# Kernel optimization log

Hardware: AMD Instinct MI355X
Metric: run time of the kernel (lower is better)

## Reference

```python
import jax, jax.numpy as jnp
import numpy as np

L = 4096
E = 512   # embed dim
S = 1024  # state dim
H = 150   # Scorer hidden dim
GI = 2 * S + E
MAX_N = 10


def _scorer(x, W1, b1, W2, b2, W3, b3):
    h = jax.nn.relu(x @ W1 + b1)
    h = jax.nn.relu(h @ W2 + b2)
    return h @ W3 + b3  # [..., 1]


def setup_inputs() -> dict:
    key = jax.random.key(0)
    ks = jax.random.split(key, 16)
    def init(k, shape, fan_in):
        return jax.random.normal(k, shape, dtype=jnp.float32) / np.sqrt(fan_in)
    inp = {
        "embeds": jax.random.normal(ks[0], (L, E), dtype=jnp.float32),
        "states": jax.random.normal(ks[1], (L, S), dtype=jnp.float32),
        # attention Scorer params (input S)
        "aW1": init(ks[2], (S, H), S), "ab1": jnp.zeros((H,), jnp.float32),
        "aW2": init(ks[3], (H, H), H), "ab2": jnp.zeros((H,), jnp.float32),
        "aW3": init(ks[4], (H, 1), H), "ab3": jnp.zeros((1,), jnp.float32),
        # sm Scorer params (input GI)
        "sW1": init(ks[5], (GI, H), GI), "sb1": jnp.zeros((H,), jnp.float32),
        "sW2": init(ks[6], (H, H), H), "sb2": jnp.zeros((H,), jnp.float32),
        "sW3": init(ks[7], (H, 1), H), "sb3": jnp.zeros((1,), jnp.float32),
    }
    return inp


def reference(embeds, states, aW1, ab1, aW2, ab2, aW3, ab3,
              sW1, sb1, sW2, sb2, sW3, sb3):
    # per-token attention logits, computed once: [L]
    attns = _scorer(states, aW1, ab1, aW2, ab2, aW3, ab3)[:, 0]

    gs = []
    for n in range(1, MAX_N + 1):  # fixed small loop over window sizes
        M = L - n + 1                                  # number of windows
        starts = jnp.arange(M)
        idx = starts[:, None] + jnp.arange(n)          # [M, n] token indices
        w = jax.nn.softmax(attns[idx], axis=1)         # windowed softmax [M, n]
        pooled = jnp.einsum('mn,mne->me', w, embeds[idx])  # [M, E]
        g = jnp.concatenate([states[starts], states[starts + n - 1], pooled],
                            axis=1)                    # [M, 2S+E]
        gs.append(g)
    x = jnp.concatenate(gs, axis=0)                    # [T, GI], T = 10L-45
    scores = _scorer(x, sW1, sb1, sW2, sb2, sW3, sb3)[:, 0]  # [T]
    return scores
```

## Files before the change

kernel.cpp:

```cpp
#include <hip/hip_runtime.h>
#include <math.h>

#define LTOK 4096
#define EDIM 512
#define SDIM 1024
#define HDIM 150
#define SEG 160
#define MAXN 10
#define TOTAL_ROWS 40915
#define KA 1536
#define NKT 48
#define K2 160
#define NCG 42

typedef _Float16 hfrag __attribute__((ext_vector_type(8)));
typedef float ffrag __attribute__((ext_vector_type(4)));


#define ITEMS_A   (LTOK * (KA / 8))
#define ITEMS_W   (NCG * NKT * 64)
#define ITEMS_W2  (K2 * (K2 / 8))
#define ITEMS_A2  (K2 * (K2 / 8))
#define ITEMS_TOT (ITEMS_A + ITEMS_W + ITEMS_W2 + ITEMS_A2)

__global__ __launch_bounds__(256) void prep_kernel(
    const float* __restrict__ embeds, const float* __restrict__ states,
    const float* __restrict__ aW1, const float* __restrict__ aW2,
    const float* __restrict__ sW1, const float* __restrict__ sW2,
    _Float16* __restrict__ Apk, _Float16* __restrict__ Wpk,
    _Float16* __restrict__ W2pk, _Float16* __restrict__ A2pk)
{
    int it = blockIdx.x * 256 + threadIdx.x;
    if (it < ITEMS_A) {
        const int rem = it % (NKT * 64);
        const int g = it / (NKT * 64), kt = rem >> 6, lane = rem & 63;
        const int row = g * 16 + (lane & 15);
        const int k0 = kt * 32 + (lane >> 4) * 8;
        const float* src = (k0 < SDIM) ? (states + (size_t)row * SDIM + k0)
                                       : (embeds + (size_t)row * EDIM + (k0 - SDIM));
        const float4 v0 = *(const float4*)src;
        const float4 v1 = *(const float4*)(src + 4);
        _Float16 o[8] = {(_Float16)v0.x, (_Float16)v0.y, (_Float16)v0.z, (_Float16)v0.w,
                         (_Float16)v1.x, (_Float16)v1.y, (_Float16)v1.z, (_Float16)v1.w};
        *(uint4*)(Apk + (size_t)it * 8) = *(uint4*)o;
        return;
    }
    it -= ITEMS_A;
    if (it < ITEMS_W) {
        const int rem = it % (NKT * 64);
        const int cgi = it / (NKT * 64), kt = rem >> 6, lane = rem & 63;
        const int col = cgi * 16 + (lane & 15);
        const int k0 = kt * 32 + (lane >> 4) * 8;
        _Float16 o[8];
        for (int j = 0; j < 8; ++j) {
            const int k = k0 + j;
            float wv = 0.f;
            if (col < 160) {
                if (col < HDIM && k < SDIM) wv = sW1[(size_t)k * HDIM + col];
            } else if (col < 320) {
                const int cj = col - 160;
                if (cj < HDIM && k < SDIM) wv = sW1[(size_t)(SDIM + k) * HDIM + cj];
            } else if (col < 480) {
                const int cj = col - 320;
                if (cj < HDIM && k >= SDIM) wv = sW1[(size_t)(SDIM + k) * HDIM + cj];
            } else if (col >= 512) {
                const int cj = col - 512;
                if (cj < HDIM && k < SDIM) wv = aW1[(size_t)k * HDIM + cj];
            }
            o[j] = (_Float16)wv;
        }
        *(uint4*)(Wpk + ((size_t)((size_t)cgi * NKT + kt) * 64 + lane) * 8) = *(uint4*)o;
        return;
    }
    it -= ITEMS_W;
    if (it < ITEMS_W2 + ITEMS_A2) {
        const bool is_a = (it >= ITEMS_W2);
        const int li = is_a ? (it - ITEMS_W2) : it;
        const float* src = is_a ? aW2 : sW2;
        _Float16* dst = is_a ? A2pk : W2pk;
        const int tk = li >> 6, lane = li & 63;
        const int col = (tk / 5) * 16 + (lane & 15);
        const int k0 = (tk % 5) * 32 + (lane >> 4) * 8;
        _Float16 o[8];
        for (int j = 0; j < 8; ++j) {
            const int k = k0 + j;
            float wv = (col < HDIM && k < HDIM) ? src[(size_t)k * HDIM + col] : 0.f;
            o[j] = (_Float16)wv;
        }
        *(uint4*)(dst + ((size_t)tk * 64 + lane) * 8) = *(uint4*)o;
    }
}

__global__ __launch_bounds__(256) void k_proj(
    const _Float16* __restrict__ Apk, const _Float16* __restrict__ Wpk,
    const _Float16* __restrict__ A2pk,
    const float* __restrict__ ab1, const float* __restrict__ ab2,
    const float* __restrict__ aW3, const float* __restrict__ ab3,
    _Float16* __restrict__ P1h, _Float16* __restrict__ P2h,
    _Float16* __restrict__ PEh, float* __restrict__ attns)
{
    const int bid = blockIdx.x;
    const int tid = threadIdx.x;
    const int w = tid >> 6, lane = tid & 63;
    const int quad = lane >> 4, l16 = lane & 15;

    __shared__ __align__(16) _Float16 smem[64 * SEG];

    if (bid % 9 == 0) {
        _Float16* ah1 = smem;
        const int tok0 = (bid / 9) * 64;
        const int g = tok0 / 16 + w;

        ffrag acc[10];
#pragma unroll
        for (int c = 0; c < 10; ++c) acc[c] = (ffrag){0.f, 0.f, 0.f, 0.f};

        const _Float16* ap = Apk + ((size_t)g * NKT) * 512 + lane * 8;
#pragma unroll 2
        for (int kt = 0; kt < 32; ++kt) {
            const hfrag a = *(const hfrag*)(ap + (size_t)kt * 512);
#pragma unroll
            for (int c = 0; c < 10; ++c) {
                const hfrag b = *(const hfrag*)(
                    Wpk + (((size_t)(32 + c) * NKT + kt) * 64 + lane) * 8);
                acc[c] = __builtin_amdgcn_mfma_f32_16x16x32_f16(a, b, acc[c], 0, 0, 0);
            }
        }
#pragma unroll
        for (int c = 0; c < 10; ++c) {
            const int col = c * 16 + l16;
            const float b1 = (col < HDIM) ? ab1[col] : 0.f;
#pragma unroll
            for (int r = 0; r < 4; ++r) {
                const int row = w * 16 + quad * 4 + r;
                ah1[row * SEG + col] = (_Float16)fmaxf(acc[c][r] + b1, 0.f);
            }
        }
        __syncthreads();

        hfrag af[5];
#pragma unroll
        for (int ks = 0; ks < 5; ++ks)
            af[ks] = *(const hfrag*)&ah1[(w * 16 + l16) * SEG + ks * 32 + quad * 8];

        float part[4] = {0.f, 0.f, 0.f, 0.f};
        for (int ct = 0; ct < 10; ++ct) {
            ffrag a2 = (ffrag){0.f, 0.f, 0.f, 0.f};
#pragma unroll
            for (int ks = 0; ks < 5; ++ks) {
                const hfrag fb = *(const hfrag*)(
                    A2pk + ((size_t)(ct * 5 + ks) * 64 + lane) * 8);
                a2 = __builtin_amdgcn_mfma_f32_16x16x32_f16(af[ks], fb, a2, 0, 0, 0);
            }
            const int col = ct * 16 + l16;
            const float s2 = (col < HDIM) ? ab2[col] : 0.f;
            const float s3 = (col < HDIM) ? aW3[col] : 0.f;
#pragma unroll
            for (int r = 0; r < 4; ++r) part[r] += fmaxf(a2[r] + s2, 0.f) * s3;
        }
#pragma unroll
        for (int off = 1; off < 16; off <<= 1) {
#pragma unroll
            for (int r = 0; r < 4; ++r) part[r] += __shfl_xor(part[r], off, 64);
        }
        if (l16 == 0) {
            const float b3 = ab3[0];
#pragma unroll
            for (int r = 0; r < 4; ++r)
                attns[tok0 + w * 16 + quad * 4 + r] = part[r] + b3;
        }
        return;
    }

    const int tile = bid - bid / 9 - 1;
    const int bM = tile & 63, bN = tile >> 6;
    const int wm = w & 1, wn = w >> 1;
    const int gbase0 = bM * 4;
    const int cgbase0 = bN * 4;
    const int cgbase = cgbase0 + wn * 2;
    const bool alive = (cgbase < 30);
    const int kt0 = (bN >= 5) ? 32 : 0;
    const int kt1 = (bN >= 5) ? 48 : 32;

    _Float16* As = smem;
    _Float16* Bs = smem + 4096;

    const int sgrp = tid >> 6, sln = tid & 63;
    const _Float16* aSrc = Apk + (((size_t)(gbase0 + sgrp) * NKT) * 64 + sln) * 8;
    const _Float16* bSrc = Wpk + (((size_t)(cgbase0 + sgrp) * NKT) * 64 + sln) * 8;
    const int sOff = (sgrp * 64 + sln) * 8;

    ffrag acc[2][2];
#pragma unroll
    for (int t = 0; t < 2; ++t)
#pragma unroll
        for (int u = 0; u < 2; ++u) acc[t][u] = (ffrag){0.f, 0.f, 0.f, 0.f};

    const int aOff0 = ((wm * 2 + 0) * 64 + lane) * 8;
    const int aOff1 = ((wm * 2 + 1) * 64 + lane) * 8;
    const int bOff0 = ((wn * 2 + 0) * 64 + lane) * 8;
    const int bOff1 = ((wn * 2 + 1) * 64 + lane) * 8;

    {
        const uint4 va = *(const uint4*)(aSrc + (size_t)kt0 * 512);
        const uint4 vb = *(const uint4*)(bSrc + (size_t)kt0 * 512);
        *(uint4*)(As + sOff) = va;
        *(uint4*)(Bs + sOff) = vb;
    }
    uint4 qa, qb;
    if (kt0 + 1 < kt1) {
        qa = *(const uint4*)(aSrc + (size_t)(kt0 + 1) * 512);
        qb = *(const uint4*)(bSrc + (size_t)(kt0 + 1) * 512);
    }
    __syncthreads();

    int buf = 0;
    for (int kt = kt0; kt < kt1; ++kt) {
        uint4 na, nb;
        const bool have2 = (kt + 2 < kt1);
        const bool have1 = (kt + 1 < kt1);
        if (have2) {
            na = *(const uint4*)(aSrc + (size_t)(kt + 2) * 512);
            nb = *(const uint4*)(bSrc + (size_t)(kt + 2) * 512);
        }
        if (have1) {
            *(uint4*)(As + (buf ^ 1) * 2048 + sOff) = qa;
            *(uint4*)(Bs + (buf ^ 1) * 2048 + sOff) = qb;
        }
        const _Float16* Ab = As + buf * 2048;
        const _Float16* Bb = Bs + buf * 2048;
        const hfrag a0 = *(const hfrag*)(Ab + aOff0);
        const hfrag a1 = *(const hfrag*)(Ab + aOff1);
        const hfrag b0 = *(const hfrag*)(Bb + bOff0);
        const hfrag b1 = *(const hfrag*)(Bb + bOff1);
        acc[0][0] = __builtin_amdgcn_mfma_f32_16x16x32_f16(a0, b0, acc[0][0], 0, 0, 0);
        acc[1][0] = __builtin_amdgcn_mfma_f32_16x16x32_f16(a1, b0, acc[1][0], 0, 0, 0);
        acc[0][1] = __builtin_amdgcn_mfma_f32_16x16x32_f16(a0, b1, acc[0][1], 0, 0, 0);
        acc[1][1] = __builtin_amdgcn_mfma_f32_16x16x32_f16(a1, b1, acc[1][1], 0, 0, 0);
        __syncthreads();
        qa = na; qb = nb;
        buf ^= 1;
    }

    if (alive) {
#pragma unroll
        for (int t = 0; t < 2; ++t)
#pragma unroll
            for (int u = 0; u < 2; ++u) {
                const int col = (cgbase + u) * 16 + l16;
#pragma unroll
                for (int r = 0; r < 4; ++r) {
                    const int row = (gbase0 + wm * 2 + t) * 16 + quad * 4 + r;
                    const _Float16 hv = (_Float16)acc[t][u][r];
                    if (col < 160)      P1h[(size_t)row * SEG + col] = hv;
                    else if (col < 320) P2h[(size_t)row * SEG + (col - 160)] = hv;
                    else if (col < 480) PEh[(size_t)row * SEG + (col - 320)] = hv;
                }
            }
    }
}

__global__ __launch_bounds__(256) void span_kernel(
    const float* __restrict__ attns, const _Float16* __restrict__ P1h,
    const _Float16* __restrict__ P2h, const _Float16* __restrict__ PEh,
    const float* __restrict__ sb1, const _Float16* __restrict__ W2pk,
    const float* __restrict__ sb2, const float* __restrict__ sW3,
    const float* __restrict__ sb3, float* __restrict__ out)
{
    const int pairI = blockIdx.x % 5;
    const int mChunk = blockIdx.x / 5;
    const int n0 = 2 * pairI + 1, n1 = n0 + 1;
    const int Mn0 = LTOK - n0 + 1, Mn1 = Mn0 - 1;
    const int m0 = mChunk * 32;
    const int offn0 = (n0 - 1) * LTOK - ((n0 - 1) * (n0 - 2)) / 2;
    const int offn1 = offn0 + Mn0;

    const int tid = threadIdx.x;
    const int w = tid >> 6, lane = tid & 63, quad = lane >> 4, l16 = lane & 15;

    __shared__ __align__(16) _Float16 h1h[2][32 * K2];
    __shared__ float wgt[2][32][MAXN];

    if (tid < 64) {
        const int q = tid >> 5, r = tid & 31;
        const int n = q ? n1 : n0;
        const int Mn = q ? Mn1 : Mn0;
        const int m = m0 + r;
        if (m < Mn) {
            float av[MAXN];
#pragma unroll
            for (int j = 0; j < MAXN; ++j)
                av[j] = attns[min(m + j, LTOK - 1)];
            float mx = -1e30f;
            for (int j = 0; j < n; ++j) mx = fmaxf(mx, av[j]);
            float tp[MAXN]; float s = 0.f;
            for (int j = 0; j < n; ++j) { tp[j] = expf(av[j] - mx); s += tp[j]; }
            const float inv = 1.f / s;
            for (int j = 0; j < MAXN; ++j) wgt[q][r][j] = (j < n) ? tp[j] * inv : 0.f;
        } else {
            for (int j = 0; j < MAXN; ++j) wgt[q][r][j] = 0.f;
        }
    }
    __syncthreads();

    for (int item = tid; item < 32 * (K2 / 8); item += 256) {
        const int r = item / (K2 / 8), cc = item % (K2 / 8);
        const int c0 = cc * 8;
        const int mm = m0 + r;
        const hfrag p1  = *(const hfrag*)(P1h + (size_t)mm * SEG + c0);
        const hfrag p2a = *(const hfrag*)(P2h + (size_t)min(mm + n0 - 1, LTOK - 1) * SEG + c0);
        const hfrag p2b = *(const hfrag*)(P2h + (size_t)min(mm + n0, LTOK - 1) * SEG + c0);
        float b1v[8];
#pragma unroll
        for (int e = 0; e < 8; ++e)
            b1v[e] = (c0 + e < HDIM) ? sb1[c0 + e] : 0.f;
        float a0[8], a1[8];
#pragma unroll
        for (int e = 0; e < 8; ++e) {
            a0[e] = (float)p1[e] + (float)p2a[e] + b1v[e];
            a1[e] = (float)p1[e] + (float)p2b[e] + b1v[e];
        }
#pragma unroll
        for (int j = 0; j < MAXN; ++j) {
            const int mj = min(mm + j, LTOK - 1);
            const hfrag pe = *(const hfrag*)(PEh + (size_t)mj * SEG + c0);
            const float w0j = wgt[0][r][j];
            const float w1j = wgt[1][r][j];
#pragma unroll
            for (int e = 0; e < 8; ++e) {
                const float pv = (float)pe[e];
                a0[e] = fmaf(w0j, pv, a0[e]);
                a1[e] = fmaf(w1j, pv, a1[e]);
            }
        }
        _Float16 o0[8], o1[8];
#pragma unroll
        for (int e = 0; e < 8; ++e) {
            const bool live = (c0 + e < HDIM);
            o0[e] = live ? (_Float16)fmaxf(a0[e], 0.f) : (_Float16)0.f;
            o1[e] = live ? (_Float16)fmaxf(a1[e], 0.f) : (_Float16)0.f;
        }
        *(uint4*)&h1h[0][r * K2 + c0] = *(uint4*)o0;
        *(uint4*)&h1h[1][r * K2 + c0] = *(uint4*)o1;
    }
    __syncthreads();

    const int q = w >> 1, rg = w & 1;
    const int Mq = q ? Mn1 : Mn0;
    const int offq = q ? offn1 : offn0;

    hfrag af[5];
#pragma unroll
    for (int ks = 0; ks < 5; ++ks)
        af[ks] = *(const hfrag*)&h1h[q][(rg * 16 + l16) * K2 + ks * 32 + quad * 8];

    float part[4] = {0.f, 0.f, 0.f, 0.f};
    for (int ct = 0; ct < 10; ++ct) {
        ffrag acc = (ffrag){0.f, 0.f, 0.f, 0.f};
#pragma unroll
        for (int ks = 0; ks < 5; ++ks) {
            const hfrag fb = *(const hfrag*)(
                W2pk + ((size_t)(ct * 5 + ks) * 64 + lane) * 8);
            acc = __builtin_amdgcn_mfma_f32_16x16x32_f16(af[ks], fb, acc, 0, 0, 0);
        }
        const int col = ct * 16 + l16;
        const float s2 = (col < HDIM) ? sb2[col] : 0.f;
        const float s3 = (col < HDIM) ? sW3[col] : 0.f;
#pragma unroll
        for (int r = 0; r < 4; ++r) part[r] += fmaxf(acc[r] + s2, 0.f) * s3;
    }

#pragma unroll
    for (int off = 1; off < 16; off <<= 1) {
#pragma unroll
        for (int r = 0; r < 4; ++r) part[r] += __shfl_xor(part[r], off, 64);
    }
    if (l16 == 0) {
        const float b3 = sb3[0];
#pragma unroll
        for (int r = 0; r < 4; ++r) {
            const int lr = rg * 16 + quad * 4 + r;
            if (m0 + lr < Mq) out[offq + m0 + lr] = part[r] + b3;
        }
    }
}

extern "C" void kernel_launch(void* const* d_in, const int* in_sizes, int n_in,
                              void* d_out, int out_size, void* d_ws, size_t ws_size,
                              hipStream_t stream) {
    const float* embeds = (const float*)d_in[0];
    const float* states = (const float*)d_in[1];
    const float* aW1 = (const float*)d_in[2];
    const float* ab1 = (const float*)d_in[3];
    const float* aW2 = (const float*)d_in[4];
    const float* ab2 = (const float*)d_in[5];
    const float* aW3 = (const float*)d_in[6];
    const float* ab3 = (const float*)d_in[7];
    const float* sW1 = (const float*)d_in[8];
    const float* sb1 = (const float*)d_in[9];
    const float* sW2 = (const float*)d_in[10];
    const float* sb2 = (const float*)d_in[11];
    const float* sW3 = (const float*)d_in[12];
    const float* sb3 = (const float*)d_in[13];
    float* out = (float*)d_out;

    float* attns = (float*)d_ws;
    _Float16* P1h  = (_Float16*)(attns + LTOK);
    _Float16* P2h  = P1h + (size_t)LTOK * SEG;
    _Float16* PEh  = P2h + (size_t)LTOK * SEG;
    _Float16* Apk  = PEh + (size_t)LTOK * SEG;
    _Float16* Wpk  = Apk + (size_t)ITEMS_A * 8;
    _Float16* W2pk = Wpk + (size_t)ITEMS_W * 8;
    _Float16* A2pk = W2pk + (size_t)ITEMS_W2 * 8;

    prep_kernel<<<ITEMS_TOT / 256, 256, 0, stream>>>(
        embeds, states, aW1, aW2, sW1, sW2, Apk, Wpk, W2pk, A2pk);
    k_proj<<<576, 256, 0, stream>>>(
        Apk, Wpk, A2pk, ab1, ab2, aW3, ab3, P1h, P2h, PEh, attns);
    span_kernel<<<640, 256, 0, stream>>>(
        attns, P1h, P2h, PEh, sb1, W2pk, sb2, sW3, sb3, out);
}
```

Measured before the change: 145.9 us.

## Fuse activation fp16 conversion into projection GEMM and stage PE rows in LDS

Drops the pre-packing of states/embeds into an fp16 MFMA layout in prep_kernel. The projection kernel now reads fp32 activations directly and converts them to fp16 while loading its tiles, which removes a full write and re-read of the packed activation buffer. The span kernel also stages the 41 PE rows each block needs into shared memory, so the 10-tap window sum reads LDS instead of repeated global loads. In exchange the GEMM loads twice the bytes per A fragment from global memory, with less coalesced strided row reads, and the span kernel uses more shared memory, which may lower occupancy.

```diff
diff --git a/kernel.cpp b/kernel.cpp
--- a/kernel.cpp
+++ b/kernel.cpp
@@ -17,35 +17,18 @@
 typedef float ffrag __attribute__((ext_vector_type(4)));
 
 
-#define ITEMS_A   (LTOK * (KA / 8))
 #define ITEMS_W   (NCG * NKT * 64)
 #define ITEMS_W2  (K2 * (K2 / 8))
 #define ITEMS_A2  (K2 * (K2 / 8))
-#define ITEMS_TOT (ITEMS_A + ITEMS_W + ITEMS_W2 + ITEMS_A2)
+#define ITEMS_PREP (ITEMS_W + ITEMS_W2 + ITEMS_A2)
 
 __global__ __launch_bounds__(256) void prep_kernel(
-    const float* __restrict__ embeds, const float* __restrict__ states,
     const float* __restrict__ aW1, const float* __restrict__ aW2,
     const float* __restrict__ sW1, const float* __restrict__ sW2,
-    _Float16* __restrict__ Apk, _Float16* __restrict__ Wpk,
-    _Float16* __restrict__ W2pk, _Float16* __restrict__ A2pk)
+    _Float16* __restrict__ Wpk, _Float16* __restrict__ W2pk,
+    _Float16* __restrict__ A2pk)
 {
     int it = blockIdx.x * 256 + threadIdx.x;
-    if (it < ITEMS_A) {
-        const int rem = it % (NKT * 64);
-        const int g = it / (NKT * 64), kt = rem >> 6, lane = rem & 63;
-        const int row = g * 16 + (lane & 15);
-        const int k0 = kt * 32 + (lane >> 4) * 8;
-        const float* src = (k0 < SDIM) ? (states + (size_t)row * SDIM + k0)
-                                       : (embeds + (size_t)row * EDIM + (k0 - SDIM));
-        const float4 v0 = *(const float4*)src;
-        const float4 v1 = *(const float4*)(src + 4);
-        _Float16 o[8] = {(_Float16)v0.x, (_Float16)v0.y, (_Float16)v0.z, (_Float16)v0.w,
-                         (_Float16)v1.x, (_Float16)v1.y, (_Float16)v1.z, (_Float16)v1.w};
-        *(uint4*)(Apk + (size_t)it * 8) = *(uint4*)o;
-        return;
-    }
-    it -= ITEMS_A;
     if (it < ITEMS_W) {
         const int rem = it % (NKT * 64);
         const int cgi = it / (NKT * 64), kt = rem >> 6, lane = rem & 63;
@@ -92,8 +75,8 @@
 }
 
 __global__ __launch_bounds__(256) void k_proj(
-    const _Float16* __restrict__ Apk, const _Float16* __restrict__ Wpk,
-    const _Float16* __restrict__ A2pk,
+    const float* __restrict__ states, const float* __restrict__ embeds,
+    const _Float16* __restrict__ Wpk, const _Float16* __restrict__ A2pk,
     const float* __restrict__ ab1, const float* __restrict__ ab2,
     const float* __restrict__ aW3, const float* __restrict__ ab3,
     _Float16* __restrict__ P1h, _Float16* __restrict__ P2h,
@@ -109,16 +92,21 @@
     if (bid % 9 == 0) {
         _Float16* ah1 = smem;
         const int tok0 = (bid / 9) * 64;
-        const int g = tok0 / 16 + w;
 
         ffrag acc[10];
 #pragma unroll
         for (int c = 0; c < 10; ++c) acc[c] = (ffrag){0.f, 0.f, 0.f, 0.f};
 
-        const _Float16* ap = Apk + ((size_t)g * NKT) * 512 + lane * 8;
+        const float* ap = states + (size_t)(tok0 + w * 16 + l16) * SDIM + quad * 8;
 #pragma unroll 2
         for (int kt = 0; kt < 32; ++kt) {
-            const hfrag a = *(const hfrag*)(ap + (size_t)kt * 512);
+            const float4 v0 = *(const float4*)(ap + kt * 32);
+            const float4 v1 = *(const float4*)(ap + kt * 32 + 4);
+            hfrag a;
+            a[0] = (_Float16)v0.x; a[1] = (_Float16)v0.y;
+            a[2] = (_Float16)v0.z; a[3] = (_Float16)v0.w;
+            a[4] = (_Float16)v1.x; a[5] = (_Float16)v1.y;
+            a[6] = (_Float16)v1.z; a[7] = (_Float16)v1.w;
 #pragma unroll
             for (int c = 0; c < 10; ++c) {
                 const hfrag b = *(const hfrag*)(
@@ -186,7 +174,10 @@
     _Float16* Bs = smem + 4096;
 
     const int sgrp = tid >> 6, sln = tid & 63;
-    const _Float16* aSrc = Apk + (((size_t)(gbase0 + sgrp) * NKT) * 64 + sln) * 8;
+    const int srow = (gbase0 + sgrp) * 16 + (sln & 15);
+    const int skcol = (sln >> 4) * 8;
+    const float* aRowS = states + (size_t)srow * SDIM;
+    const float* aRowE = embeds + (size_t)srow * EDIM;
     const _Float16* bSrc = Wpk + (((size_t)(cgbase0 + sgrp) * NKT) * 64 + sln) * 8;
     const int sOff = (sgrp * 64 + sln) * 8;
 
@@ -201,30 +192,46 @@
     const int bOff0 = ((wn * 2 + 0) * 64 + lane) * 8;
     const int bOff1 = ((wn * 2 + 1) * 64 + lane) * 8;
 
+#define A_LOAD(kt, d0, d1)                                                  \
+    {                                                                       \
+        const int k0_ = (kt) * 32 + skcol;                                  \
+        const float* s_ = (k0_ < SDIM) ? (aRowS + k0_)                      \
+                                       : (aRowE + (k0_ - SDIM));            \
+        d0 = *(const float4*)s_;                                            \
+        d1 = *(const float4*)(s_ + 4);                                      \
+    }
+#define A_STORE(buf_, d0, d1)                                               \
+    {                                                                       \
+        _Float16 o_[8] = {(_Float16)d0.x, (_Float16)d0.y, (_Float16)d0.z,   \
+                          (_Float16)d0.w, (_Float16)d1.x, (_Float16)d1.y,   \
+                          (_Float16)d1.z, (_Float16)d1.w};                  \
+        *(uint4*)(As + (buf_) * 2048 + sOff) = *(uint4*)o_;                 \
+    }
+
     {
-        const uint4 va = *(const uint4*)(aSrc + (size_t)kt0 * 512);
-        const uint4 vb = *(const uint4*)(bSrc + (size_t)kt0 * 512);
-        *(uint4*)(As + sOff) = va;
-        *(uint4*)(Bs + sOff) = vb;
-    }
-    uint4 qa, qb;
+        float4 p0, p1;
+        A_LOAD(kt0, p0, p1);
+        A_STORE(0, p0, p1);
+        *(uint4*)(Bs + sOff) = *(const uint4*)(bSrc + (size_t)kt0 * 512);
+    }
+    float4 qa0, qa1; uint4 qb;
     if (kt0 + 1 < kt1) {
-        qa = *(const uint4*)(aSrc + (size_t)(kt0 + 1) * 512);
+        A_LOAD(kt0 + 1, qa0, qa1);
         qb = *(const uint4*)(bSrc + (size_t)(kt0 + 1) * 512);
     }
     __syncthreads();
 
     int buf = 0;
     for (int kt = kt0; kt < kt1; ++kt) {
-        uint4 na, nb;
+        float4 na0, na1; uint4 nb;
         const bool have2 = (kt + 2 < kt1);
         const bool have1 = (kt + 1 < kt1);
         if (have2) {
-            na = *(const uint4*)(aSrc + (size_t)(kt + 2) * 512);
+            A_LOAD(kt + 2, na0, na1);
             nb = *(const uint4*)(bSrc + (size_t)(kt + 2) * 512);
         }
         if (have1) {
-            *(uint4*)(As + (buf ^ 1) * 2048 + sOff) = qa;
+            A_STORE(buf ^ 1, qa0, qa1);
             *(uint4*)(Bs + (buf ^ 1) * 2048 + sOff) = qb;
         }
         const _Float16* Ab = As + buf * 2048;
@@ -238,9 +245,11 @@
         acc[0][1] = __builtin_amdgcn_mfma_f32_16x16x32_f16(a0, b1, acc[0][1], 0, 0, 0);
         acc[1][1] = __builtin_amdgcn_mfma_f32_16x16x32_f16(a1, b1, acc[1][1], 0, 0, 0);
         __syncthreads();
-        qa = na; qb = nb;
+        qa0 = na0; qa1 = na1; qb = nb;
         buf ^= 1;
     }
+#undef A_LOAD
+#undef A_STORE
 
     if (alive) {
 #pragma unroll
@@ -279,7 +288,15 @@
     const int w = tid >> 6, lane = tid & 63, quad = lane >> 4, l16 = lane & 15;
 
     __shared__ __align__(16) _Float16 h1h[2][32 * K2];
+    __shared__ __align__(16) _Float16 PEs[41 * SEG];
     __shared__ float wgt[2][32][MAXN];
+
+    for (int t = tid; t < 41 * (SEG / 8); t += 256) {
+        const int rr = t / (SEG / 8), cc = t % (SEG / 8);
+        const int srcRow = min(m0 + rr, LTOK - 1);
+        *(uint4*)&PEs[rr * SEG + cc * 8] =
+            *(const uint4*)(PEh + (size_t)srcRow * SEG + cc * 8);
+    }
 
     if (tid < 64) {
         const int q = tid >> 5, r = tid & 31;
@@ -322,8 +339,7 @@
         }
 #pragma unroll
         for (int j = 0; j < MAXN; ++j) {
-            const int mj = min(mm + j, LTOK - 1);
-            const hfrag pe = *(const hfrag*)(PEh + (size_t)mj * SEG + c0);
+            const hfrag pe = *(const hfrag*)&PEs[(r + j) * SEG + c0];
             const float w0j = wgt[0][r][j];
             const float w1j = wgt[1][r][j];
 #pragma unroll
@@ -408,15 +424,14 @@
     _Float16* P1h  = (_Float16*)(attns + LTOK);
     _Float16* P2h  = P1h + (size_t)LTOK * SEG;
     _Float16* PEh  = P2h + (size_t)LTOK * SEG;
-    _Float16* Apk  = PEh + (size_t)LTOK * SEG;
-    _Float16* Wpk  = Apk + (size_t)ITEMS_A * 8;
+    _Float16* Wpk  = PEh + (size_t)LTOK * SEG;
     _Float16* W2pk = Wpk + (size_t)ITEMS_W * 8;
     _Float16* A2pk = W2pk + (size_t)ITEMS_W2 * 8;
 
-    prep_kernel<<<ITEMS_TOT / 256, 256, 0, stream>>>(
-        embeds, states, aW1, aW2, sW1, sW2, Apk, Wpk, W2pk, A2pk);
+    prep_kernel<<<ITEMS_PREP / 256, 256, 0, stream>>>(
+        aW1, aW2, sW1, sW2, Wpk, W2pk, A2pk);
     k_proj<<<576, 256, 0, stream>>>(
-        Apk, Wpk, A2pk, ab1, ab2, aW3, ab3, P1h, P2h, PEh, attns);
+        states, embeds, Wpk, A2pk, ab1, ab2, aW3, ab3, P1h, P2h, PEh, attns);
     span_kernel<<<640, 256, 0, stream>>>(
         attns, P1h, P2h, PEh, sb1, W2pk, sb2, sW3, sb3, out);
 }
```

Result: slower. 156.4 us (+7.2%).
